# Optimization experiments

Hardware: AMD Instinct MI355X
Metric: run time of the kernel (lower is better)

Reference implementation:

```python
import jax, jax.numpy as jnp
import numpy as np

TEMP = 0.07
EPS = 1e-8
NUM_CLASSES = 7
THRESH = 0.3


def setup_inputs() -> dict:
    key = jax.random.key(0)
    k1, k2, k3, k4, k5 = jax.random.split(key, 5)
    N, H, E, C = 8192, 128, 256, NUM_CLASSES
    reps = jax.random.normal(k1, (N, H), dtype=jnp.float32)
    labels = jax.random.randint(k2, (N,), 0, C, dtype=jnp.int64 if jax.config.jax_enable_x64 else jnp.int32)
    centers = jax.random.normal(k3, (C, E), dtype=jnp.float32)
    fc_w = jax.random.normal(k4, (H, E), dtype=jnp.float32) * (1.0 / np.sqrt(E))
    fc_b = jax.random.normal(k5, (H,), dtype=jnp.float32) * 0.01
    return {"reps": reps, "labels": labels, "centers": centers, "fc_w": fc_w, "fc_b": fc_b}


def reference(reps, labels, centers, fc_w, fc_b):
    # fc(default_centers): [C, H]
    curr_centers = centers @ fc_w.T + fc_b
    pad_labels = jnp.arange(NUM_CLASSES, dtype=labels.dtype)

    all_reps = jnp.concatenate([reps, curr_centers], axis=0)      # [M, H]
    all_labels = jnp.concatenate([labels, pad_labels], axis=0)    # [M]
    B = reps.shape[0]
    M = all_reps.shape[0]

    # cosine similarity via normalized matmul (avoids [B,M,H] broadcast)
    norms = jnp.sqrt(jnp.sum(all_reps * all_reps, axis=-1))
    rn = all_reps / jnp.maximum(norms, 1e-8)[:, None]
    cos = rn[:B] @ rn.T                                           # [B, M]

    scores = (1.0 + cos) * 0.5 + EPS
    eye = (jnp.arange(B)[:, None] == jnp.arange(M)[None, :]).astype(scores.dtype)
    scores = scores * (1.0 - eye) / TEMP
    # torch uses .item() on the max -> a non-differentiable constant
    scores = scores - jax.lax.stop_gradient(jnp.max(scores))
    e = jnp.exp(scores)

    pos_mask = (labels[:, None] == all_labels[None, :]).astype(scores.dtype)  # [B, M]
    mask = 1.0 - eye

    pos_sum = jnp.sum(e * pos_mask * mask, axis=-1)
    neg_sum = jnp.sum(e * (1.0 - pos_mask), axis=-1)
    probs = pos_sum / (pos_sum + neg_sum)
    probs = probs / (jnp.sum(pos_mask * mask, axis=-1) + EPS)

    loss_vec = -jnp.log(probs + EPS)
    loss_mask = (loss_vec > THRESH).astype(loss_vec.dtype)
    denom = jax.lax.stop_gradient(jnp.sum(loss_mask)) + EPS
    loss = jnp.sum(loss_vec * loss_mask) / denom
    return loss
```

## Files before the change

kernel.cpp:

```cpp
#include <hip/hip_runtime.h>
#include <hip/hip_bf16.h>

#define BN 8192
#define MM 8199
#define MP 8208
#define HH 128
#define EE 256
#define NTILE 513
#define JCH 32

typedef __attribute__((ext_vector_type(8))) short short8;
typedef __attribute__((ext_vector_type(4))) float floatx4;

__global__ __launch_bounds__(64)
void centers_kernel(const float* __restrict__ centers,
                    const float* __restrict__ fc_w,
                    const float* __restrict__ fc_b,
                    float* __restrict__ curr) {
  int o = blockIdx.x;
  int c = o >> 7, h = o & 127;
  int lane = threadIdx.x;
  const float4* ce = (const float4*)(centers + c * EE);
  const float4* w  = (const float4*)(fc_w + h * EE);
  float4 a = ce[lane];
  float4 b = w[lane];
  float s = a.x * b.x + a.y * b.y + a.z * b.z + a.w * b.w;
#pragma unroll
  for (int m = 1; m < 64; m <<= 1) s += __shfl_xor(s, m);
  if (lane == 0) curr[o] = s + fc_b[h];
}

__global__ __launch_bounds__(64)
void norm_kernel(const float* __restrict__ reps,
                 const float* __restrict__ curr,
                 const int* __restrict__ labels,
                 __hip_bfloat16* __restrict__ rn,
                 int* __restrict__ labp) {
  int r = blockIdx.x;
  int lane = threadIdx.x;
  float2 v = make_float2(0.f, 0.f);
  if (r < BN)      v = ((const float2*)(reps + (size_t)r * HH))[lane];
  else if (r < MM) v = ((const float2*)(curr + (size_t)(r - BN) * HH))[lane];
  float ss = v.x * v.x + v.y * v.y;
#pragma unroll
  for (int m = 1; m < 64; m <<= 1) ss += __shfl_xor(ss, m);
  float inv = 1.0f / fmaxf(sqrtf(ss), 1e-8f);
  __hip_bfloat162 h2;
  h2.x = __float2bfloat16(v.x * inv);
  h2.y = __float2bfloat16(v.y * inv);
  ((__hip_bfloat162*)(rn + (size_t)r * HH))[lane] = h2;
  if (lane == 0) labp[r] = (r < BN) ? labels[r] : (r < MM ? r - BN : -1);
}

__global__ __launch_bounds__(64)
void main_kernel(const __hip_bfloat16* __restrict__ rn,
                 const int* __restrict__ labp,
                 float* __restrict__ tot,
                 float* __restrict__ pos) {
  const int lane = threadIdx.x;
  const int q = lane >> 4, col = lane & 15;
  const int ibase = blockIdx.x * 64;
  const short* rns = (const short*)rn;

  short8 afrag[4][4];
#pragma unroll
  for (int it = 0; it < 4; ++it) {
    const short8* p = (const short8*)(rns + (size_t)(ibase + it * 16 + col) * HH + q * 8);
    afrag[it][0] = p[0];
    afrag[it][1] = p[4];
    afrag[it][2] = p[8];
    afrag[it][3] = p[12];
  }
  int labi[4][4];
#pragma unroll
  for (int it = 0; it < 4; ++it)
#pragma unroll
    for (int r = 0; r < 4; ++r)
      labi[it][r] = labp[ibase + it * 16 + q * 4 + r];

  float stot[4][4] = {};
  float spos[4][4] = {};
  const float K2 = 10.30496147f;

  for (int t = blockIdx.y; t < NTILE; t += JCH) {
    const int jb = t * 16;
    const int jg = jb + col;
    const short8* bp = (const short8*)(rns + (size_t)jg * HH + q * 8);
    short8 b0 = bp[0], b1 = bp[4], b2 = bp[8], b3 = bp[12];
    const int labj = labp[jg];
    const float jvf = (jg < MM) ? 1.f : 0.f;
#pragma unroll
    for (int it = 0; it < 4; ++it) {
      floatx4 acc = {0.f, 0.f, 0.f, 0.f};
      acc = __builtin_amdgcn_mfma_f32_16x16x32_bf16(afrag[it][0], b0, acc, 0, 0, 0);
      acc = __builtin_amdgcn_mfma_f32_16x16x32_bf16(afrag[it][1], b1, acc, 0, 0, 0);
      acc = __builtin_amdgcn_mfma_f32_16x16x32_bf16(afrag[it][2], b2, acc, 0, 0, 0);
      acc = __builtin_amdgcn_mfma_f32_16x16x32_bf16(afrag[it][3], b3, acc, 0, 0, 0);
      const bool isdiag = (jb == ibase + it * 16);
#pragma unroll
      for (int r = 0; r < 4; ++r) {
        float e = exp2f(fmaf(acc[r], K2, -K2)) * jvf;
        if (isdiag && (col == q * 4 + r)) e = 0.f;
        stot[it][r] += e;
        spos[it][r] += (labj == labi[it][r]) ? e : 0.f;
      }
    }
  }

#pragma unroll
  for (int it = 0; it < 4; ++it)
#pragma unroll
    for (int r = 0; r < 4; ++r) {
      float tt = stot[it][r], pp = spos[it][r];
#pragma unroll
      for (int m = 1; m <= 8; m <<= 1) {
        tt += __shfl_xor(tt, m);
        pp += __shfl_xor(pp, m);
      }
      if (col == 0) {
        int i = ibase + it * 16 + q * 4 + r;
        atomicAdd(&tot[i], tt);
        atomicAdd(&pos[i], pp);
      }
    }
}

__global__ __launch_bounds__(256)
void loss_kernel(const float* __restrict__ tot,
                 const float* __restrict__ pos,
                 const int* __restrict__ labels,
                 float* __restrict__ out) {
  __shared__ int hist[8];
  __shared__ float s1[256], s2[256];
  int tid = threadIdx.x;
  if (tid < 8) hist[tid] = 0;
  __syncthreads();
  for (int i = tid; i < BN; i += 256) atomicAdd(&hist[labels[i]], 1);
  __syncthreads();
  float lsum = 0.f, msum = 0.f;
  for (int i = tid; i < BN; i += 256) {
    float t = tot[i], p = pos[i];
    float c = (float)hist[labels[i]];
    float pr = (p / t) / (c + 1e-8f);
    float lv = -logf(pr + 1e-8f);
    if (lv > 0.3f) { lsum += lv; msum += 1.f; }
  }
  s1[tid] = lsum; s2[tid] = msum;
  __syncthreads();
  for (int st = 128; st > 0; st >>= 1) {
    if (tid < st) { s1[tid] += s1[tid + st]; s2[tid] += s2[tid + st]; }
    __syncthreads();
  }
  if (tid == 0) out[0] = s1[0] / (s2[0] + 1e-8f);
}

extern "C" void kernel_launch(void* const* d_in, const int* in_sizes, int n_in,
                              void* d_out, int out_size, void* d_ws, size_t ws_size,
                              hipStream_t stream) {
  const float* reps    = (const float*)d_in[0];
  const int*   labels  = (const int*)d_in[1];
  const float* centers = (const float*)d_in[2];
  const float* fc_w    = (const float*)d_in[3];
  const float* fc_b    = (const float*)d_in[4];
  float* out = (float*)d_out;

  char* ws = (char*)d_ws;
  float* curr = (float*)ws;
  int* labp   = (int*)(ws + 4096);
  __hip_bfloat16* rn = (__hip_bfloat16*)(ws + 40960);
  float* tot = (float*)(ws + 40960 + 2101248);
  float* pos = tot + BN;

  hipMemsetAsync(tot, 0, 2 * BN * sizeof(float), stream);
  centers_kernel<<<896, 64, 0, stream>>>(centers, fc_w, fc_b, curr);
  norm_kernel<<<MP, 64, 0, stream>>>(reps, curr, labels, rn, labp);
  main_kernel<<<dim3(128, JCH), 64, 0, stream>>>(rn, labp, tot, pos);
  loss_kernel<<<1, 256, 0, stream>>>(tot, pos, labels, out);
}
```

Baseline: 145.0 us.

## Pack four waves per block, drop pad mask, and parallelise loss reduction

```diff
diff --git a/kernel.cpp b/kernel.cpp
--- a/kernel.cpp
+++ b/kernel.cpp
@@ -7,19 +7,20 @@
 #define HH 128
 #define EE 256
 #define NTILE 513
-#define JCH 32
+#define JCHUNKS 64
+#define NUM_HIST 7
 
 typedef __attribute__((ext_vector_type(8))) short short8;
 typedef __attribute__((ext_vector_type(4))) float floatx4;
 
-__global__ __launch_bounds__(64)
+__global__ __launch_bounds__(256)
 void centers_kernel(const float* __restrict__ centers,
                     const float* __restrict__ fc_w,
                     const float* __restrict__ fc_b,
                     float* __restrict__ curr) {
-  int o = blockIdx.x;
+  int wid = threadIdx.x >> 6, lane = threadIdx.x & 63;
+  int o = (blockIdx.x << 2) | wid;
   int c = o >> 7, h = o & 127;
-  int lane = threadIdx.x;
   const float4* ce = (const float4*)(centers + c * EE);
   const float4* w  = (const float4*)(fc_w + h * EE);
   float4 a = ce[lane];
@@ -30,14 +31,14 @@
   if (lane == 0) curr[o] = s + fc_b[h];
 }
 
-__global__ __launch_bounds__(64)
+__global__ __launch_bounds__(256)
 void norm_kernel(const float* __restrict__ reps,
                  const float* __restrict__ curr,
                  const int* __restrict__ labels,
                  __hip_bfloat16* __restrict__ rn,
                  int* __restrict__ labp) {
-  int r = blockIdx.x;
-  int lane = threadIdx.x;
+  int wid = threadIdx.x >> 6, lane = threadIdx.x & 63;
+  int r = (blockIdx.x << 2) | wid;
   float2 v = make_float2(0.f, 0.f);
   if (r < BN)      v = ((const float2*)(reps + (size_t)r * HH))[lane];
   else if (r < MM) v = ((const float2*)(curr + (size_t)(r - BN) * HH))[lane];
@@ -52,14 +53,16 @@
   if (lane == 0) labp[r] = (r < BN) ? labels[r] : (r < MM ? r - BN : -1);
 }
 
-__global__ __launch_bounds__(64)
+__global__ __launch_bounds__(256, 5)
 void main_kernel(const __hip_bfloat16* __restrict__ rn,
                  const int* __restrict__ labp,
                  float* __restrict__ tot,
                  float* __restrict__ pos) {
-  const int lane = threadIdx.x;
+  const int lane = threadIdx.x & 63;
+  const int wid  = threadIdx.x >> 6;
   const int q = lane >> 4, col = lane & 15;
   const int ibase = blockIdx.x * 64;
+  const int chunk = (blockIdx.y << 2) | wid;
   const short* rns = (const short*)rn;
 
   short8 afrag[4][4];
@@ -82,13 +85,17 @@
   float spos[4][4] = {};
   const float K2 = 10.30496147f;
 
-  for (int t = blockIdx.y; t < NTILE; t += JCH) {
-    const int jb = t * 16;
-    const int jg = jb + col;
-    const short8* bp = (const short8*)(rns + (size_t)jg * HH + q * 8);
-    short8 b0 = bp[0], b1 = bp[4], b2 = bp[8], b3 = bp[12];
-    const int labj = labp[jg];
-    const float jvf = (jg < MM) ? 1.f : 0.f;
+  const short* bptr = rns + (chunk * 16 + col) * HH + q * 8;
+  const int* lptr = labp + chunk * 16 + col;
+
+  for (int jb = chunk * 16; jb < MP; jb += 16 * JCHUNKS) {
+    short8 b0 = ((const short8*)bptr)[0];
+    short8 b1 = ((const short8*)bptr)[4];
+    short8 b2 = ((const short8*)bptr)[8];
+    short8 b3 = ((const short8*)bptr)[12];
+    const int labj = *lptr;
+    bptr += 16 * JCHUNKS * HH;
+    lptr += 16 * JCHUNKS;
 #pragma unroll
     for (int it = 0; it < 4; ++it) {
       floatx4 acc = {0.f, 0.f, 0.f, 0.f};
@@ -99,7 +106,7 @@
       const bool isdiag = (jb == ibase + it * 16);
 #pragma unroll
       for (int r = 0; r < 4; ++r) {
-        float e = exp2f(fmaf(acc[r], K2, -K2)) * jvf;
+        float e = exp2f(fmaf(acc[r], K2, -K2));
         if (isdiag && (col == q * 4 + r)) e = 0.f;
         stot[it][r] += e;
         spos[it][r] += (labj == labi[it][r]) ? e : 0.f;
@@ -125,33 +132,68 @@
     }
 }
 
-__global__ __launch_bounds__(256)
+__global__ __launch_bounds__(1024)
 void loss_kernel(const float* __restrict__ tot,
                  const float* __restrict__ pos,
                  const int* __restrict__ labels,
                  float* __restrict__ out) {
-  __shared__ int hist[8];
-  __shared__ float s1[256], s2[256];
-  int tid = threadIdx.x;
-  if (tid < 8) hist[tid] = 0;
+  __shared__ int hist[NUM_HIST];
+  __shared__ float s1[16], s2[16];
+  const int tid = threadIdx.x;
+  const int lane = tid & 63, wid = tid >> 6;
+  if (tid < NUM_HIST) hist[tid] = 0;
   __syncthreads();
-  for (int i = tid; i < BN; i += 256) atomicAdd(&hist[labels[i]], 1);
+  int cnt0 = 0, cnt1 = 0, cnt2 = 0, cnt3 = 0, cnt4 = 0, cnt5 = 0, cnt6 = 0;
+  for (int i = tid; i < BN; i += 1024) {
+    int lab = labels[i];
+    unsigned long long m0 = __ballot(lab == 0);
+    unsigned long long m1 = __ballot(lab == 1);
+    unsigned long long m2 = __ballot(lab == 2);
+    unsigned long long m3 = __ballot(lab == 3);
+    unsigned long long m4 = __ballot(lab == 4);
+    unsigned long long m5 = __ballot(lab == 5);
+    unsigned long long m6 = __ballot(lab == 6);
+    if (lane == 0) {
+      cnt0 += __popcll(m0); cnt1 += __popcll(m1); cnt2 += __popcll(m2);
+      cnt3 += __popcll(m3); cnt4 += __popcll(m4); cnt5 += __popcll(m5);
+      cnt6 += __popcll(m6);
+    }
+  }
+  if (lane == 0) {
+    atomicAdd(&hist[0], cnt0); atomicAdd(&hist[1], cnt1);
+    atomicAdd(&hist[2], cnt2); atomicAdd(&hist[3], cnt3);
+    atomicAdd(&hist[4], cnt4); atomicAdd(&hist[5], cnt5);
+    atomicAdd(&hist[6], cnt6);
+  }
   __syncthreads();
+  const float K2 = 10.30496147f;
+  const float epad = exp2f(-K2);
   float lsum = 0.f, msum = 0.f;
-  for (int i = tid; i < BN; i += 256) {
-    float t = tot[i], p = pos[i];
+  for (int i = tid; i < BN; i += 1024) {
+    float t = tot[i] - 9.0f * epad;
+    float p = pos[i];
     float c = (float)hist[labels[i]];
     float pr = (p / t) / (c + 1e-8f);
     float lv = -logf(pr + 1e-8f);
     if (lv > 0.3f) { lsum += lv; msum += 1.f; }
   }
-  s1[tid] = lsum; s2[tid] = msum;
+#pragma unroll
+  for (int m = 1; m < 64; m <<= 1) {
+    lsum += __shfl_xor(lsum, m);
+    msum += __shfl_xor(msum, m);
+  }
+  if (lane == 0) { s1[wid] = lsum; s2[wid] = msum; }
   __syncthreads();
-  for (int st = 128; st > 0; st >>= 1) {
-    if (tid < st) { s1[tid] += s1[tid + st]; s2[tid] += s2[tid + st]; }
-    __syncthreads();
-  }
-  if (tid == 0) out[0] = s1[0] / (s2[0] + 1e-8f);
+  if (wid == 0) {
+    float a = (lane < 16) ? s1[lane] : 0.f;
+    float b = (lane < 16) ? s2[lane] : 0.f;
+#pragma unroll
+    for (int m = 1; m < 16; m <<= 1) {
+      a += __shfl_xor(a, m);
+      b += __shfl_xor(b, m);
+    }
+    if (lane == 0) out[0] = a / (b + 1e-8f);
+  }
 }
 
 extern "C" void kernel_launch(void* const* d_in, const int* in_sizes, int n_in,
@@ -172,8 +214,8 @@
   float* pos = tot + BN;
 
   hipMemsetAsync(tot, 0, 2 * BN * sizeof(float), stream);
-  centers_kernel<<<896, 64, 0, stream>>>(centers, fc_w, fc_b, curr);
-  norm_kernel<<<MP, 64, 0, stream>>>(reps, curr, labels, rn, labp);
-  main_kernel<<<dim3(128, JCH), 64, 0, stream>>>(rn, labp, tot, pos);
-  loss_kernel<<<1, 256, 0, stream>>>(tot, pos, labels, out);
-}
+  centers_kernel<<<224, 256, 0, stream>>>(centers, fc_w, fc_b, curr);
+  norm_kernel<<<2052, 256, 0, stream>>>(reps, curr, labels, rn, labp);
+  main_kernel<<<dim3(128, 16), 256, 0, stream>>>(rn, labp, tot, pos);
+  loss_kernel<<<1, 1024, 0, stream>>>(tot, pos, labels, out);
+}
```

New measurement: 263.6 us. 81.7% more time.
